# Optimization experiments

Hardware: AMD Instinct MI355X
Metric: run time of the kernel (lower is better)

## Reference

```python
import jax, jax.numpy as jnp
import numpy as np
from functools import partial

H = 1024  # hidden_sz
B, T = 32, 256
NL = 4    # stacked LSTM layers
WSCALE = 0.02


def setup_inputs() -> dict:
    key = jax.random.key(0)
    ks = jax.random.split(key, 8)
    x = jax.random.normal(ks[0], (B, T, H), dtype=jnp.float32)
    h0 = jnp.zeros((B, H), dtype=jnp.float32)
    c0 = jnp.zeros((B, H), dtype=jnp.float32)
    # LSTM params per layer: kernel [H,4H], recurrent kernel [H,4H], bias [4H]
    Wk = jax.random.normal(ks[1], (NL, H, 4 * H), dtype=jnp.float32) * WSCALE
    Wr = jax.random.normal(ks[2], (NL, H, 4 * H), dtype=jnp.float32) * WSCALE
    b = jnp.zeros((NL, 4 * H), dtype=jnp.float32)
    # dense head
    Wd = jax.random.normal(ks[3], (H, H), dtype=jnp.float32) * WSCALE
    bd = jnp.zeros((H,), dtype=jnp.float32)
    return {"x": x, "h0": h0, "c0": c0, "Wk": Wk, "Wr": Wr, "b": b, "Wd": Wd, "bd": bd}


def _lstm_layer(x_tbd, h0, c0, Wk, Wr, b):
    # Keras LSTM with activation='relu', recurrent_activation='sigmoid'.
    # Gate order in keras kernels: i, f, c(candidate), o.
    xw = jnp.einsum('tbd,dg->tbg', x_tbd, Wk) + b  # precompute input projections [T,B,4H]

    def step(carry, xw_t):
        h, c = carry
        z = xw_t + h @ Wr  # [B,4H]
        i, f, g, o = jnp.split(z, 4, axis=-1)
        i = jax.nn.sigmoid(i)
        f = jax.nn.sigmoid(f)
        o = jax.nn.sigmoid(o)
        c = f * c + i * jax.nn.relu(g)
        h = o * jax.nn.relu(c)
        return (h, c), h

    (hT, cT), hs = jax.lax.scan(step, (h0, c0), xw)
    return hs, hT, cT  # hs: [T,B,H]


def reference(x, h0, c0, Wk, Wr, b, Wd, bd):
    # x: [B,T,H] -> time-major [T,B,H]
    seq = jnp.transpose(x, (1, 0, 2))
    h, c = h0, c0
    for l in range(NL):
        seq, h, c = _lstm_layer(seq, h, c, Wk[l], Wr[l], b[l])
        # dropout layers are identity at inference (training=False)
    out = jnp.einsum('tbh,hd->tbd', seq, Wd) + bd
    out = jnp.transpose(out, (1, 0, 2))  # back to [B,T,H]
    return out, h, c
```

## Files before the change

kernel.cpp:

```cpp
#include <hip/hip_runtime.h>

#define TT 256
#define BB 32
#define HH 1024
#define GG 4096

typedef __attribute__((ext_vector_type(8))) short short8;
typedef __attribute__((ext_vector_type(4))) float f32x4;

__device__ __forceinline__ unsigned short rne_bf16(float x) {
    unsigned u = __float_as_uint(x);
    unsigned r = (u + 0x7FFFu + ((u >> 16) & 1u)) >> 16;
    return (unsigned short)r;
}
__device__ __forceinline__ float bf16f(unsigned short s) {
    return __uint_as_float((unsigned)s << 16);
}

__global__ __launch_bounds__(256) void k_transpose(const float* __restrict__ x, float* __restrict__ seq) {
    int idx = blockIdx.x * 256 + threadIdx.x;
    int k4 = idx & 255;
    int tb = idx >> 8;
    int t = tb >> 5, b = tb & 31;
    float4 v = ((const float4*)x)[((size_t)b * TT + t) * 256 + k4];
    ((float4*)seq)[(size_t)tb * 256 + k4] = v;
}

__global__ __launch_bounds__(256) void k_init_hc(const float* __restrict__ h0, const float* __restrict__ c0,
                                                 float* __restrict__ h, float* __restrict__ c) {
    int i = blockIdx.x * 256 + threadIdx.x;
    ((float4*)h)[i] = ((const float4*)h0)[i];
    ((float4*)c)[i] = ((const float4*)c0)[i];
}

__global__ __launch_bounds__(256) void k_copy_hc(const float* __restrict__ h, const float* __restrict__ c,
                                                 float* __restrict__ oh, float* __restrict__ oc) {
    int i = blockIdx.x * 256 + threadIdx.x;
    ((float4*)oh)[i] = ((const float4*)h)[i];
    ((float4*)oc)[i] = ((const float4*)c)[i];
}

__global__ __launch_bounds__(256) void k_wrt(const float* __restrict__ Wr, float* __restrict__ WrT) {
    __shared__ float tile[64][65];
    int c0 = blockIdx.x * 64;
    int k0 = blockIdx.y * 64;
    int tid = threadIdx.x;
    int tr = tid >> 4, tc4 = tid & 15;
#pragma unroll
    for (int p = 0; p < 4; ++p) {
        int r = p * 16 + tr;
        float4 v = *(const float4*)&Wr[(size_t)(k0 + r) * GG + c0 + tc4 * 4];
        tile[r][tc4 * 4 + 0] = v.x;
        tile[r][tc4 * 4 + 1] = v.y;
        tile[r][tc4 * 4 + 2] = v.z;
        tile[r][tc4 * 4 + 3] = v.w;
    }
    __syncthreads();
#pragma unroll
    for (int p = 0; p < 4; ++p) {
        int cc = p * 16 + tr;
        float4 v;
        v.x = tile[tc4 * 4 + 0][cc];
        v.y = tile[tc4 * 4 + 1][cc];
        v.z = tile[tc4 * 4 + 2][cc];
        v.w = tile[tc4 * 4 + 3][cc];
        *(float4*)&WrT[(size_t)(c0 + cc) * 1024 + k0 + tc4 * 4] = v;
    }
}

__global__ __launch_bounds__(256) void k_wkt3(const float* __restrict__ Wk, unsigned short* __restrict__ W1,
                                              unsigned short* __restrict__ W2, unsigned short* __restrict__ W3) {
    __shared__ float tile[64][65];
    int c0 = blockIdx.x * 64;
    int k0 = blockIdx.y * 64;
    int tid = threadIdx.x;
    int tr = tid >> 4, tc4 = tid & 15;
#pragma unroll
    for (int p = 0; p < 4; ++p) {
        int r = p * 16 + tr;
        float4 v = *(const float4*)&Wk[(size_t)(k0 + r) * GG + c0 + tc4 * 4];
        tile[r][tc4 * 4 + 0] = v.x;
        tile[r][tc4 * 4 + 1] = v.y;
        tile[r][tc4 * 4 + 2] = v.z;
        tile[r][tc4 * 4 + 3] = v.w;
    }
    __syncthreads();
#pragma unroll
    for (int p = 0; p < 4; ++p) {
        int cc = p * 16 + tr;
        ushort4 o1, o2, o3;
        unsigned short* po1 = (unsigned short*)&o1;
        unsigned short* po2 = (unsigned short*)&o2;
        unsigned short* po3 = (unsigned short*)&o3;
#pragma unroll
        for (int e = 0; e < 4; ++e) {
            float v = tile[tc4 * 4 + e][cc];
            unsigned short s1 = rne_bf16(v);
            float r1 = v - bf16f(s1);
            unsigned short s2 = rne_bf16(r1);
            float r2 = r1 - bf16f(s2);
            unsigned short s3 = rne_bf16(r2);
            po1[e] = s1; po2[e] = s2; po3[e] = s3;
        }
        size_t off = (size_t)(c0 + cc) * 1024 + k0 + tc4 * 4;
        *(ushort4*)&W1[off] = o1;
        *(ushort4*)&W2[off] = o2;
        *(ushort4*)&W3[off] = o3;
    }
}

__global__ __launch_bounds__(256, 2) void k_gemm_mx3(const float* __restrict__ A,
                                                     const unsigned short* __restrict__ B1,
                                                     const unsigned short* __restrict__ B2,
                                                     const unsigned short* __restrict__ B3,
                                                     const float* __restrict__ bias, float* __restrict__ C) {
    __shared__ unsigned short Asl[3][6144];
    __shared__ unsigned short Bsl[3][6144];
    int tid = threadIdx.x;
    int m0 = blockIdx.x * 128, n0 = blockIdx.y * 128;
    int lane = tid & 63, wv = tid >> 6;
    int wr = (wv >> 1) * 64, wc = (wv & 1) * 64;
    int l15 = lane & 15, ko = (lane >> 4) * 8;

    f32x4 acc[4][4];
#pragma unroll
    for (int i = 0; i < 4; ++i)
#pragma unroll
        for (int j = 0; j < 4; ++j) acc[i][j] = (f32x4){0.f, 0.f, 0.f, 0.f};

    const unsigned short* Bg[3] = {B1, B2, B3};

    for (int k0 = 0; k0 < 1024; k0 += 32) {
#pragma unroll
        for (int i = 0; i < 4; ++i) {
            int idx = i * 256 + tid;
            int m = idx >> 3, kq = idx & 7;
            float4 v = *(const float4*)&A[(size_t)(m0 + m) * 1024 + k0 + kq * 4];
            float xs[4] = {v.x, v.y, v.z, v.w};
            ushort4 o1, o2, o3;
            unsigned short* po1 = (unsigned short*)&o1;
            unsigned short* po2 = (unsigned short*)&o2;
            unsigned short* po3 = (unsigned short*)&o3;
#pragma unroll
            for (int e = 0; e < 4; ++e) {
                unsigned short s1 = rne_bf16(xs[e]);
                float r1 = xs[e] - bf16f(s1);
                unsigned short s2 = rne_bf16(r1);
                float r2 = r1 - bf16f(s2);
                unsigned short s3 = rne_bf16(r2);
                po1[e] = s1; po2[e] = s2; po3[e] = s3;
            }
            int loff = m * 48 + kq * 4;
            *(ushort4*)&Asl[0][loff] = o1;
            *(ushort4*)&Asl[1][loff] = o2;
            *(ushort4*)&Asl[2][loff] = o3;
        }
#pragma unroll
        for (int sp = 0; sp < 3; ++sp) {
            const unsigned short* bg = Bg[sp];
#pragma unroll
            for (int i = 0; i < 2; ++i) {
                int idx = i * 256 + tid;
                int n = idx >> 2, kq = idx & 3;
                short8 v = *(const short8*)&bg[(size_t)(n0 + n) * 1024 + k0 + kq * 8];
                *(short8*)&Bsl[sp][n * 48 + kq * 8] = v;
            }
        }
        __syncthreads();

        short8 af[3][4];
#pragma unroll
        for (int mi = 0; mi < 4; ++mi) {
            int ro = (wr + mi * 16 + l15) * 48 + ko;
#pragma unroll
            for (int sp = 0; sp < 3; ++sp) af[sp][mi] = *(const short8*)&Asl[sp][ro];
        }
#pragma unroll
        for (int ni = 0; ni < 4; ++ni) {
            int co = (wc + ni * 16 + l15) * 48 + ko;
            short8 b0 = *(const short8*)&Bsl[0][co];
            short8 b1 = *(const short8*)&Bsl[1][co];
            short8 b2 = *(const short8*)&Bsl[2][co];
#pragma unroll
            for (int mi = 0; mi < 4; ++mi) {
                f32x4 a = acc[mi][ni];
                a = __builtin_amdgcn_mfma_f32_16x16x32_bf16(af[0][mi], b0, a, 0, 0, 0);
                a = __builtin_amdgcn_mfma_f32_16x16x32_bf16(af[1][mi], b0, a, 0, 0, 0);
                a = __builtin_amdgcn_mfma_f32_16x16x32_bf16(af[0][mi], b1, a, 0, 0, 0);
                a = __builtin_amdgcn_mfma_f32_16x16x32_bf16(af[2][mi], b0, a, 0, 0, 0);
                a = __builtin_amdgcn_mfma_f32_16x16x32_bf16(af[1][mi], b1, a, 0, 0, 0);
                a = __builtin_amdgcn_mfma_f32_16x16x32_bf16(af[0][mi], b2, a, 0, 0, 0);
                acc[mi][ni] = a;
            }
        }
        __syncthreads();
    }

#pragma unroll
    for (int ni = 0; ni < 4; ++ni) {
        int col = n0 + wc + ni * 16 + l15;
        float bv = bias[col];
#pragma unroll
        for (int mi = 0; mi < 4; ++mi) {
            int rbase = m0 + wr + mi * 16 + (lane >> 4) * 4;
#pragma unroll
            for (int r = 0; r < 4; ++r)
                C[(size_t)(rbase + r) * 4096 + col] = acc[mi][ni][r] + bv;
        }
    }
}

template <int MODE>
__global__ __launch_bounds__(256) void k_gemm(const float* __restrict__ A, const float* __restrict__ W,
                                              const float* __restrict__ bias, float* __restrict__ C, int N) {
    __shared__ float As[16][132];
    __shared__ float Bs[16][132];
    const int K = 1024;
    int tid = threadIdx.x;
    int m0 = blockIdx.x * 128, n0 = blockIdx.y * 128;
    int tx = tid & 15, ty = tid >> 4;
    int a_row = tid >> 2, a_kq = tid & 3;
    int b_cq = tid & 31, b_k = tid >> 5;
    float acc[8][8];
#pragma unroll
    for (int i = 0; i < 8; ++i)
#pragma unroll
        for (int jj = 0; jj < 8; ++jj) acc[i][jj] = 0.f;

    for (int kc = 0; kc < K; kc += 16) {
#pragma unroll
        for (int it = 0; it < 2; ++it) {
            int row = a_row + it * 64;
            float4 v = *(const float4*)&A[(size_t)(m0 + row) * K + kc + a_kq * 4];
            As[a_kq * 4 + 0][row] = v.x;
            As[a_kq * 4 + 1][row] = v.y;
            As[a_kq * 4 + 2][row] = v.z;
            As[a_kq * 4 + 3][row] = v.w;
        }
#pragma unroll
        for (int it = 0; it < 2; ++it) {
            int kk = b_k + it * 8;
            float4 v = *(const float4*)&W[(size_t)(kc + kk) * N + n0 + b_cq * 4];
            *(float4*)&Bs[kk][b_cq * 4] = v;
        }
        __syncthreads();
#pragma unroll
        for (int kk = 0; kk < 16; ++kk) {
            float4 a0 = *(const float4*)&As[kk][ty * 8];
            float4 a1 = *(const float4*)&As[kk][ty * 8 + 4];
            float4 b0 = *(const float4*)&Bs[kk][tx * 8];
            float4 b1 = *(const float4*)&Bs[kk][tx * 8 + 4];
            float am[8] = {a0.x, a0.y, a0.z, a0.w, a1.x, a1.y, a1.z, a1.w};
            float bv[8] = {b0.x, b0.y, b0.z, b0.w, b1.x, b1.y, b1.z, b1.w};
#pragma unroll
            for (int i = 0; i < 8; ++i)
#pragma unroll
                for (int jj = 0; jj < 8; ++jj) acc[i][jj] += am[i] * bv[jj];
        }
        __syncthreads();
    }
#pragma unroll
    for (int i = 0; i < 8; ++i) {
        int m = m0 + ty * 8 + i;
#pragma unroll
        for (int jj = 0; jj < 8; jj += 4) {
            int n = n0 + tx * 8 + jj;
            float4 v;
            v.x = acc[i][jj + 0] + bias[n + 0];
            v.y = acc[i][jj + 1] + bias[n + 1];
            v.z = acc[i][jj + 2] + bias[n + 2];
            v.w = acc[i][jj + 3] + bias[n + 3];
            if (MODE == 0) {
                *(float4*)&C[(size_t)m * N + n] = v;
            } else {
                int t = m >> 5, b = m & 31;
                *(float4*)&C[((size_t)b * TT + t) * HH + n] = v;
            }
        }
    }
}

__global__ __launch_bounds__(512) void k_step_T3(const float* __restrict__ WrT, const float* __restrict__ xw_t,
                                                 float* __restrict__ seq_t, const float* __restrict__ h_in,
                                                 float* __restrict__ h_out, float* __restrict__ c) {
    __shared__ float h_lds[34816];
    __shared__ float zred[8][32][17];
    int tid = threadIdx.x;
    int j = tid & 15, ks = tid >> 4;
    int hc0 = blockIdx.x * 4;
    int col = (j >> 2) * HH + hc0 + (j & 3);

    const float4* WrT4 = (const float4*)WrT;
    int wbase = col * 256 + ks * 8;
    float4 w[8];
#pragma unroll
    for (int q = 0; q < 8; ++q) w[q] = WrT4[wbase + q];

    int rb = tid >> 2, rd = tid & 3;
    float pz[4];
    if (tid < 128) {
#pragma unroll
        for (int g = 0; g < 4; ++g) pz[g] = xw_t[rb * GG + g * HH + hc0 + rd];
    }

    const float4* hp4 = (const float4*)h_in;
    float4* hl4w = (float4*)h_lds;
#pragma unroll 8
    for (int it = 0; it < 16; ++it) {
        int gi = it * 512 + tid;
        float4 v = hp4[gi];
        int b = gi >> 8, kk = gi & 255;
        hl4w[b * 272 + (kk >> 4) * 17 + (kk & 15)] = v;
    }
    __syncthreads();

    const float4* hl4 = (const float4*)h_lds;
    int base4 = (ks >> 1) * 17 + (ks & 1) * 8;
    float acc[32];
#pragma unroll
    for (int b = 0; b < 32; ++b) acc[b] = 0.f;
#pragma unroll
    for (int q = 0; q < 8; ++q) {
        float4 wq = w[q];
#pragma unroll
        for (int b = 0; b < 32; ++b) {
            float4 hv = hl4[b * 272 + base4 + q];
            acc[b] += wq.x * hv.x + wq.y * hv.y + wq.z * hv.z + wq.w * hv.w;
        }
    }
#pragma unroll
    for (int b = 0; b < 32; ++b) {
        acc[b] += __shfl_xor(acc[b], 16);
        acc[b] += __shfl_xor(acc[b], 32);
    }
    int wv = tid >> 6;
    if ((ks & 3) == 0) {
#pragma unroll
        for (int b = 0; b < 32; ++b) zred[wv][b][j] = acc[b];
    }
    __syncthreads();

    if (tid < 128) {
        float zz[4];
#pragma unroll
        for (int g = 0; g < 4; ++g) {
            float s = pz[g];
#pragma unroll
            for (int u = 0; u < 8; ++u) s += zred[u][rb][g * 4 + rd];
            zz[g] = s;
        }
        float si = 1.f / (1.f + expf(-zz[0]));
        float sf = 1.f / (1.f + expf(-zz[1]));
        float gg = fmaxf(zz[2], 0.f);
        float so = 1.f / (1.f + expf(-zz[3]));
        float cv = c[rb * HH + hc0 + rd];
        cv = sf * cv + si * gg;
        c[rb * HH + hc0 + rd] = cv;
        float hn = so * fmaxf(cv, 0.f);
        h_out[rb * HH + hc0 + rd] = hn;
        seq_t[rb * HH + hc0 + rd] = hn;
    }
}

__global__ __launch_bounds__(256) void k_step(const float* __restrict__ Wr, const float* __restrict__ xw_t,
                                              float* __restrict__ seq_t, const float* __restrict__ h_in,
                                              float* __restrict__ h_out, float* __restrict__ c) {
    __shared__ float zred[4][32][17];
    int tid = threadIdx.x;
    int j = tid & 15, ks = tid >> 4;
    int hc0 = blockIdx.x * 4;
    int col = (j >> 2) * HH + hc0 + (j & 3);
    float4 w[16];
#pragma unroll
    for (int q = 0; q < 16; ++q) {
        size_t kb = (size_t)(ks * 64 + q * 4) * GG + col;
        w[q].x = Wr[kb];
        w[q].y = Wr[kb + GG];
        w[q].z = Wr[kb + 2 * (size_t)GG];
        w[q].w = Wr[kb + 3 * (size_t)GG];
    }
    const float4* hp = (const float4*)h_in;
    int kq0 = ks * 16;
    float acc[32];
#pragma unroll
    for (int b = 0; b < 32; ++b) acc[b] = 0.f;
#pragma unroll
    for (int q = 0; q < 16; ++q) {
        float4 wq = w[q];
#pragma unroll
        for (int b = 0; b < 32; ++b) {
            float4 hv = hp[b * 256 + kq0 + q];
            acc[b] += wq.x * hv.x + wq.y * hv.y + wq.z * hv.z + wq.w * hv.w;
        }
    }
#pragma unroll
    for (int b = 0; b < 32; ++b) {
        acc[b] += __shfl_xor(acc[b], 16);
        acc[b] += __shfl_xor(acc[b], 32);
    }
    int wv = tid >> 6;
    if ((ks & 3) == 0) {
#pragma unroll
        for (int b = 0; b < 32; ++b) zred[wv][b][j] = acc[b];
    }
    __syncthreads();
    if (tid < 128) {
        int rb = tid >> 2, rd = tid & 3;
        float zz[4];
#pragma unroll
        for (int g = 0; g < 4; ++g) {
            float s = xw_t[rb * GG + g * HH + hc0 + rd];
#pragma unroll
            for (int u = 0; u < 4; ++u) s += zred[u][rb][g * 4 + rd];
            zz[g] = s;
        }
        float si = 1.f / (1.f + expf(-zz[0]));
        float sf = 1.f / (1.f + expf(-zz[1]));
        float gg = fmaxf(zz[2], 0.f);
        float so = 1.f / (1.f + expf(-zz[3]));
        float cv = c[rb * HH + hc0 + rd];
        cv = sf * cv + si * gg;
        c[rb * HH + hc0 + rd] = cv;
        float hn = so * fmaxf(cv, 0.f);
        h_out[rb * HH + hc0 + rd] = hn;
        seq_t[rb * HH + hc0 + rd] = hn;
    }
}

extern "C" void kernel_launch(void* const* d_in, const int* in_sizes, int n_in,
                              void* d_out, int out_size, void* d_ws, size_t ws_size,
                              hipStream_t stream) {
    const float* x  = (const float*)d_in[0];
    const float* h0 = (const float*)d_in[1];
    const float* c0 = (const float*)d_in[2];
    const float* Wk = (const float*)d_in[3];
    const float* Wr = (const float*)d_in[4];
    const float* bs = (const float*)d_in[5];
    const float* Wd = (const float*)d_in[6];
    const float* bd = (const float*)d_in[7];
    float* out = (float*)d_out;
    float* ws  = (float*)d_ws;

    float* xw  = ws;
    float* seq = ws + 33554432;
    float* h0b = seq + 8388608;
    float* h1b = h0b + 32768;
    float* c   = h1b + 32768;
    float* wrt = c + 32768;
    const size_t base_floats = 46235648;
    unsigned short* wkt1 = (unsigned short*)(ws + base_floats);
    unsigned short* wkt2 = wkt1 + 4194304;
    unsigned short* wkt3 = wkt2 + 4194304;
    bool fast    = ws_size >= base_floats * 4;
    bool mfma_ok = ws_size >= base_floats * 4 + (size_t)3 * 4194304 * 2;

    k_transpose<<<8192, 256, 0, stream>>>(x, seq);
    k_init_hc<<<32, 256, 0, stream>>>(h0, c0, h0b, c);

    for (int l = 0; l < 4; ++l) {
        const float* Wrl = Wr + (size_t)l * 1024 * 4096;
        const float* Wkl = Wk + (size_t)l * 1024 * 4096;
        if (mfma_ok) {
            k_wkt3<<<dim3(64, 16), 256, 0, stream>>>(Wkl, wkt1, wkt2, wkt3);
            k_gemm_mx3<<<dim3(64, 32), 256, 0, stream>>>(seq, wkt1, wkt2, wkt3, bs + l * 4096, xw);
        } else {
            k_gemm<0><<<dim3(64, 32), 256, 0, stream>>>(seq, Wkl, bs + l * 4096, xw, 4096);
        }
        if (fast) k_wrt<<<dim3(64, 16), 256, 0, stream>>>(Wrl, wrt);
        for (int t = 0; t < TT; ++t) {
            const float* hin = (t & 1) ? h1b : h0b;
            float* hout      = (t & 1) ? h0b : h1b;
            if (fast)
                k_step_T3<<<256, 512, 0, stream>>>(wrt, xw + (size_t)t * (BB * GG),
                                                   seq + (size_t)t * (BB * HH), hin, hout, c);
            else
                k_step<<<256, 256, 0, stream>>>(Wrl, xw + (size_t)t * (BB * GG),
                                                seq + (size_t)t * (BB * HH), hin, hout, c);
        }
    }

    k_gemm<1><<<dim3(64, 8), 256, 0, stream>>>(seq, Wd, bd, out, 1024);
    k_copy_hc<<<32, 256, 0, stream>>>(h0b, c, out + 8388608, out + 8388608 + 32768);
}
```

Baseline: 14.90 ms.

## Compute recurrent step with bf16x3 MFMA using pre-split recurrent weights and hidden state

Adds a per-step kernel that computes h@Wr with bf16 MFMA instructions, using a three-way bf16 split of both the recurrent weights and the hidden state to keep near-fp32 accuracy. The recurrent weights are transposed, split and reordered once per layer, and each step writes the split h for the next step, so no per-step conversion of the weights is needed. The goal is to replace the scalar fp32 FMA recurrent matvec with matrix cores. It needs more workspace and falls back to the old path when the workspace is too small. Weights are now read from global/L2 in bf16 each step instead of being held in registers as fp32.

```diff
diff --git a/kernel.cpp b/kernel.cpp
--- a/kernel.cpp
+++ b/kernel.cpp
@@ -31,6 +31,33 @@
     int i = blockIdx.x * 256 + threadIdx.x;
     ((float4*)h)[i] = ((const float4*)h0)[i];
     ((float4*)c)[i] = ((const float4*)c0)[i];
+}
+
+__global__ __launch_bounds__(256) void k_init_hc2(const float* __restrict__ h0, const float* __restrict__ c0,
+                                                  float* __restrict__ h, float* __restrict__ c,
+                                                  unsigned short* __restrict__ hb1,
+                                                  unsigned short* __restrict__ hb2,
+                                                  unsigned short* __restrict__ hb3) {
+    int i = blockIdx.x * 256 + threadIdx.x;
+    float4 hv = ((const float4*)h0)[i];
+    ((float4*)h)[i] = hv;
+    ((float4*)c)[i] = ((const float4*)c0)[i];
+    float xs[4] = {hv.x, hv.y, hv.z, hv.w};
+    ushort4 o1, o2, o3;
+    unsigned short* p1 = (unsigned short*)&o1;
+    unsigned short* p2 = (unsigned short*)&o2;
+    unsigned short* p3 = (unsigned short*)&o3;
+#pragma unroll
+    for (int e = 0; e < 4; ++e) {
+        unsigned short s1 = rne_bf16(xs[e]);
+        float r1 = xs[e] - bf16f(s1);
+        unsigned short s2 = rne_bf16(r1);
+        float r2 = r1 - bf16f(s2);
+        p1[e] = s1; p2[e] = s2; p3[e] = rne_bf16(r2);
+    }
+    *(ushort4*)&hb1[i * 4] = o1;
+    *(ushort4*)&hb2[i * 4] = o2;
+    *(ushort4*)&hb3[i * 4] = o3;
 }
 
 __global__ __launch_bounds__(256) void k_copy_hc(const float* __restrict__ h, const float* __restrict__ c,
@@ -68,6 +95,45 @@
     }
 }
 
+__global__ __launch_bounds__(256) void k_wrt3(const float* __restrict__ Wr, unsigned short* __restrict__ W1,
+                                              unsigned short* __restrict__ W2, unsigned short* __restrict__ W3) {
+    __shared__ float tile[64][65];
+    int c0 = blockIdx.x * 64;
+    int k0 = blockIdx.y * 64;
+    int tid = threadIdx.x;
+    int tr = tid >> 4, tc4 = tid & 15;
+#pragma unroll
+    for (int p = 0; p < 4; ++p) {
+        int r = p * 16 + tr;
+        float4 v = *(const float4*)&Wr[(size_t)(k0 + r) * GG + c0 + tc4 * 4];
+        tile[r][tc4 * 4 + 0] = v.x;
+        tile[r][tc4 * 4 + 1] = v.y;
+        tile[r][tc4 * 4 + 2] = v.z;
+        tile[r][tc4 * 4 + 3] = v.w;
+    }
+    __syncthreads();
+    int cc = tid & 63, kq = tid >> 6;
+    int G = c0 + cc;
+    int outrow = ((G & 1023) >> 2) * 16 + (G >> 10) * 4 + (G & 3);
+    size_t obase = (size_t)outrow * 1024 + k0 + kq * 16;
+    unsigned short t1[16], t2[16], t3[16];
+#pragma unroll
+    for (int e = 0; e < 16; ++e) {
+        float v = tile[kq * 16 + e][cc];
+        unsigned short s1 = rne_bf16(v);
+        float r1 = v - bf16f(s1);
+        unsigned short s2 = rne_bf16(r1);
+        float r2 = r1 - bf16f(s2);
+        t1[e] = s1; t2[e] = s2; t3[e] = rne_bf16(r2);
+    }
+#pragma unroll
+    for (int hlf = 0; hlf < 2; ++hlf) {
+        *(short8*)&W1[obase + hlf * 8] = *(short8*)&t1[hlf * 8];
+        *(short8*)&W2[obase + hlf * 8] = *(short8*)&t2[hlf * 8];
+        *(short8*)&W3[obase + hlf * 8] = *(short8*)&t3[hlf * 8];
+    }
+}
+
 __global__ __launch_bounds__(256) void k_wkt3(const float* __restrict__ Wk, unsigned short* __restrict__ W1,
                                               unsigned short* __restrict__ W2, unsigned short* __restrict__ W3) {
     __shared__ float tile[64][65];
@@ -99,8 +165,7 @@
             float r1 = v - bf16f(s1);
             unsigned short s2 = rne_bf16(r1);
             float r2 = r1 - bf16f(s2);
-            unsigned short s3 = rne_bf16(r2);
-            po1[e] = s1; po2[e] = s2; po3[e] = s3;
+            po1[e] = s1; po2[e] = s2; po3[e] = rne_bf16(r2);
         }
         size_t off = (size_t)(c0 + cc) * 1024 + k0 + tc4 * 4;
         *(ushort4*)&W1[off] = o1;
@@ -147,8 +212,7 @@
                 float r1 = xs[e] - bf16f(s1);
                 unsigned short s2 = rne_bf16(r1);
                 float r2 = r1 - bf16f(s2);
-                unsigned short s3 = rne_bf16(r2);
-                po1[e] = s1; po2[e] = s2; po3[e] = s3;
+                po1[e] = s1; po2[e] = s2; po3[e] = rne_bf16(r2);
             }
             int loff = m * 48 + kq * 4;
             *(ushort4*)&Asl[0][loff] = o1;
@@ -280,6 +344,96 @@
     }
 }
 
+__global__ __launch_bounds__(512) void k_step_mfma(
+    const unsigned short* __restrict__ Wb1, const unsigned short* __restrict__ Wb2,
+    const unsigned short* __restrict__ Wb3,
+    const unsigned short* __restrict__ Ha1, const unsigned short* __restrict__ Ha2,
+    const unsigned short* __restrict__ Ha3,
+    unsigned short* __restrict__ Ho1, unsigned short* __restrict__ Ho2,
+    unsigned short* __restrict__ Ho3,
+    const float* __restrict__ xw_t, float* __restrict__ seq_t,
+    float* __restrict__ h_out, float* __restrict__ c) {
+    __shared__ float zs[8][16][33];
+    int tid = threadIdx.x;
+    int lane = tid & 63, wv = tid >> 6;
+    int blk = blockIdx.x;
+    int l15 = lane & 15, ko = (lane >> 4) * 8;
+
+    int rb = tid >> 2, rd = tid & 3;
+    float pz[4];
+    if (tid < 128) {
+#pragma unroll
+        for (int g = 0; g < 4; ++g) pz[g] = xw_t[rb * GG + g * HH + blk * 4 + rd];
+    }
+
+    size_t bbase  = ((size_t)blk * 16 + l15) * 1024 + ko;
+    size_t abase0 = (size_t)l15 * 1024 + ko;
+    size_t abase1 = (size_t)(16 + l15) * 1024 + ko;
+
+    f32x4 acc0 = (f32x4){0.f, 0.f, 0.f, 0.f};
+    f32x4 acc1 = (f32x4){0.f, 0.f, 0.f, 0.f};
+
+#pragma unroll
+    for (int kt = 0; kt < 4; ++kt) {
+        int kk = (wv * 4 + kt) * 32;
+        short8 b0  = *(const short8*)&Wb1[bbase + kk];
+        short8 b1  = *(const short8*)&Wb2[bbase + kk];
+        short8 b2  = *(const short8*)&Wb3[bbase + kk];
+        short8 a00 = *(const short8*)&Ha1[abase0 + kk];
+        short8 a01 = *(const short8*)&Ha2[abase0 + kk];
+        short8 a02 = *(const short8*)&Ha3[abase0 + kk];
+        short8 a10 = *(const short8*)&Ha1[abase1 + kk];
+        short8 a11 = *(const short8*)&Ha2[abase1 + kk];
+        short8 a12 = *(const short8*)&Ha3[abase1 + kk];
+        acc0 = __builtin_amdgcn_mfma_f32_16x16x32_bf16(a00, b0, acc0, 0, 0, 0);
+        acc0 = __builtin_amdgcn_mfma_f32_16x16x32_bf16(a01, b0, acc0, 0, 0, 0);
+        acc0 = __builtin_amdgcn_mfma_f32_16x16x32_bf16(a00, b1, acc0, 0, 0, 0);
+        acc0 = __builtin_amdgcn_mfma_f32_16x16x32_bf16(a02, b0, acc0, 0, 0, 0);
+        acc0 = __builtin_amdgcn_mfma_f32_16x16x32_bf16(a01, b1, acc0, 0, 0, 0);
+        acc0 = __builtin_amdgcn_mfma_f32_16x16x32_bf16(a00, b2, acc0, 0, 0, 0);
+        acc1 = __builtin_amdgcn_mfma_f32_16x16x32_bf16(a10, b0, acc1, 0, 0, 0);
+        acc1 = __builtin_amdgcn_mfma_f32_16x16x32_bf16(a11, b0, acc1, 0, 0, 0);
+        acc1 = __builtin_amdgcn_mfma_f32_16x16x32_bf16(a10, b1, acc1, 0, 0, 0);
+        acc1 = __builtin_amdgcn_mfma_f32_16x16x32_bf16(a12, b0, acc1, 0, 0, 0);
+        acc1 = __builtin_amdgcn_mfma_f32_16x16x32_bf16(a11, b1, acc1, 0, 0, 0);
+        acc1 = __builtin_amdgcn_mfma_f32_16x16x32_bf16(a10, b2, acc1, 0, 0, 0);
+    }
+
+#pragma unroll
+    for (int r = 0; r < 4; ++r) {
+        zs[wv][l15][(lane >> 4) * 4 + r]      = acc0[r];
+        zs[wv][l15][16 + (lane >> 4) * 4 + r] = acc1[r];
+    }
+    __syncthreads();
+
+    if (tid < 128) {
+        float zz[4];
+#pragma unroll
+        for (int g = 0; g < 4; ++g) {
+            float s = pz[g];
+#pragma unroll
+            for (int u = 0; u < 8; ++u) s += zs[u][g * 4 + rd][rb];
+            zz[g] = s;
+        }
+        float si = 1.f / (1.f + expf(-zz[0]));
+        float sf = 1.f / (1.f + expf(-zz[1]));
+        float gg = fmaxf(zz[2], 0.f);
+        float so = 1.f / (1.f + expf(-zz[3]));
+        int hi = rb * HH + blk * 4 + rd;
+        float cv = c[hi];
+        cv = sf * cv + si * gg;
+        c[hi] = cv;
+        float hn = so * fmaxf(cv, 0.f);
+        h_out[hi] = hn;
+        seq_t[hi] = hn;
+        unsigned short s1 = rne_bf16(hn);
+        float r1 = hn - bf16f(s1);
+        unsigned short s2 = rne_bf16(r1);
+        float r2 = r1 - bf16f(s2);
+        Ho1[hi] = s1; Ho2[hi] = s2; Ho3[hi] = rne_bf16(r2);
+    }
+}
+
 __global__ __launch_bounds__(512) void k_step_T3(const float* __restrict__ WrT, const float* __restrict__ xw_t,
                                                  float* __restrict__ seq_t, const float* __restrict__ h_in,
                                                  float* __restrict__ h_out, float* __restrict__ c) {
@@ -451,11 +605,25 @@
     unsigned short* wkt1 = (unsigned short*)(ws + base_floats);
     unsigned short* wkt2 = wkt1 + 4194304;
     unsigned short* wkt3 = wkt2 + 4194304;
-    bool fast    = ws_size >= base_floats * 4;
-    bool mfma_ok = ws_size >= base_floats * 4 + (size_t)3 * 4194304 * 2;
+    unsigned short* wrb1 = wkt3 + 4194304;
+    unsigned short* wrb2 = wrb1 + 4194304;
+    unsigned short* wrb3 = wrb2 + 4194304;
+    unsigned short* hA1  = wrb3 + 4194304;
+    unsigned short* hA2  = hA1 + 32768;
+    unsigned short* hA3  = hA2 + 32768;
+    unsigned short* hB1  = hA3 + 32768;
+    unsigned short* hB2  = hB1 + 32768;
+    unsigned short* hB3  = hB2 + 32768;
+
+    bool fast     = ws_size >= base_floats * 4;
+    bool mfma_ok  = ws_size >= base_floats * 4 + (size_t)3 * 4194304 * 2;
+    bool mfma2_ok = ws_size >= base_floats * 4 + (size_t)6 * 4194304 * 2 + 6 * 32768 * 2;
 
     k_transpose<<<8192, 256, 0, stream>>>(x, seq);
-    k_init_hc<<<32, 256, 0, stream>>>(h0, c0, h0b, c);
+    if (mfma2_ok)
+        k_init_hc2<<<32, 256, 0, stream>>>(h0, c0, h0b, c, hA1, hA2, hA3);
+    else
+        k_init_hc<<<32, 256, 0, stream>>>(h0, c0, h0b, c);
 
     for (int l = 0; l < 4; ++l) {
         const float* Wrl = Wr + (size_t)l * 1024 * 4096;
@@ -466,16 +634,32 @@
         } else {
             k_gemm<0><<<dim3(64, 32), 256, 0, stream>>>(seq, Wkl, bs + l * 4096, xw, 4096);
         }
-        if (fast) k_wrt<<<dim3(64, 16), 256, 0, stream>>>(Wrl, wrt);
-        for (int t = 0; t < TT; ++t) {
-            const float* hin = (t & 1) ? h1b : h0b;
-            float* hout      = (t & 1) ? h0b : h1b;
-            if (fast)
-                k_step_T3<<<256, 512, 0, stream>>>(wrt, xw + (size_t)t * (BB * GG),
-                                                   seq + (size_t)t * (BB * HH), hin, hout, c);
-            else
-                k_step<<<256, 256, 0, stream>>>(Wrl, xw + (size_t)t * (BB * GG),
-                                                seq + (size_t)t * (BB * HH), hin, hout, c);
+        if (mfma2_ok) {
+            k_wrt3<<<dim3(64, 16), 256, 0, stream>>>(Wrl, wrb1, wrb2, wrb3);
+            for (int t = 0; t < TT; ++t) {
+                float* hout = (t & 1) ? h0b : h1b;
+                const unsigned short* i1 = (t & 1) ? hB1 : hA1;
+                const unsigned short* i2 = (t & 1) ? hB2 : hA2;
+                const unsigned short* i3 = (t & 1) ? hB3 : hA3;
+                unsigned short* o1 = (t & 1) ? hA1 : hB1;
+                unsigned short* o2 = (t & 1) ? hA2 : hB2;
+                unsigned short* o3 = (t & 1) ? hA3 : hB3;
+                k_step_mfma<<<256, 512, 0, stream>>>(wrb1, wrb2, wrb3, i1, i2, i3, o1, o2, o3,
+                                                     xw + (size_t)t * (BB * GG),
+                                                     seq + (size_t)t * (BB * HH), hout, c);
+            }
+        } else {
+            if (fast) k_wrt<<<dim3(64, 16), 256, 0, stream>>>(Wrl, wrt);
+            for (int t = 0; t < TT; ++t) {
+                const float* hin = (t & 1) ? h1b : h0b;
+                float* hout      = (t & 1) ? h0b : h1b;
+                if (fast)
+                    k_step_T3<<<256, 512, 0, stream>>>(wrt, xw + (size_t)t * (BB * GG),
+                                                       seq + (size_t)t * (BB * HH), hin, hout, c);
+                else
+                    k_step<<<256, 256, 0, stream>>>(Wrl, xw + (size_t)t * (BB * GG),
+                                                    seq + (size_t)t * (BB * HH), hin, hout, c);
+            }
         }
     }
 
```

Result: faster. 13.48 ms, median of 2 (-9.5%).
